# Performance work log

Hardware: AMD Instinct MI355X
Metric: run time of the kernel (lower is better)

## Reference

```python
import jax, jax.numpy as jnp
import numpy as np

N = 4096
FIN = 4096
LOC = 16
H1, H2, HEADS = 120, 50, 4
H1_PER = H1 // HEADS
FILM_Z = 32
SSDB_H = 60
N_HEMI = N // 2
NEG_SLOPE = 0.1
GATE_BIAS = -2.0
MASK_FILL = -9e15


def leaky(x):
    return jax.nn.leaky_relu(x, negative_slope=NEG_SLOPE)


def gat(x, mask, W, a_src, a_dst, bias, concat):
    # x: (N, Fin), W: (H, Fin, O), a_src/a_dst: (H, O), mask: (N, N) bool
    wh = jnp.einsum('nf,hfo->hno', x, W)            # (H, N, O)
    f1 = jnp.einsum('hno,ho->hn', wh, a_src)        # (H, N)
    f2 = jnp.einsum('hno,ho->hn', wh, a_dst)        # (H, N)
    e = leaky(f1[:, :, None] + f2[:, None, :])      # (H, N, N)
    e = jnp.where(mask[None], e, MASK_FILL)
    alpha = jax.nn.softmax(e, axis=-1)
    out = jnp.einsum('hij,hjo->hio', alpha, wh)     # (H, N, O)
    if concat:
        h, n, o = out.shape
        out2 = out.transpose(1, 0, 2).reshape(n, h * o)
    else:
        out2 = out.mean(axis=0)
    return out2 + bias


def _uni(k, shape, stdv):
    return jax.random.uniform(k, shape, jnp.float32, -stdv, stdv)


def setup_inputs() -> dict:
    key = jax.random.key(0)
    ks = jax.random.split(key, 30)
    s1 = 1.0 / np.sqrt(H1_PER)
    s2 = 1.0 / np.sqrt(H2)
    inp = {
        'x_fc': jax.random.normal(ks[0], (N, FIN), jnp.float32),
        'adj': jax.random.randint(ks[1], (N, N), 0, 2, jnp.int32),
        'l_loc': jax.random.uniform(ks[2], (N, LOC), jnp.float32),
        # gat1
        'W1': _uni(ks[3], (HEADS, FIN, H1_PER), s1),
        'a1s': _uni(ks[4], (HEADS, H1_PER), s1),
        'a1d': _uni(ks[5], (HEADS, H1_PER), s1),
        'b1': _uni(ks[6], (H1,), s1),
        # gat2
        'W2': _uni(ks[7], (1, H1, H2), s2),
        'a2s': _uni(ks[8], (1, H2), s2),
        'a2d': _uni(ks[9], (1, H2), s2),
        'b2': _uni(ks[10], (H2,), s2),
        # classifier (no bias)
        'Wc': _uni(ks[11], (2, H2), s2),
        # FiLM trunk
        'Wl1': _uni(ks[12], (FILM_Z, LOC), 1.0 / np.sqrt(LOC)),
        'bl1': _uni(ks[13], (FILM_Z,), 1.0 / np.sqrt(LOC)),
        'Wl2': _uni(ks[14], (FILM_Z, FILM_Z), 1.0 / np.sqrt(FILM_Z)),
        'bl2': _uni(ks[15], (FILM_Z,), 1.0 / np.sqrt(FILM_Z)),
        'Wg': _uni(ks[16], (H2, FILM_Z), 1.0 / np.sqrt(FILM_Z)),
        'bg': _uni(ks[17], (H2,), 1.0 / np.sqrt(FILM_Z)),
        'Wb': _uni(ks[18], (H2, FILM_Z), 1.0 / np.sqrt(FILM_Z)),
        'bb': _uni(ks[19], (H2,), 1.0 / np.sqrt(FILM_Z)),
        'Wgate': _uni(ks[20], (1, FILM_Z), 1.0 / np.sqrt(FILM_Z)),
        'bgate': jnp.full((1,), GATE_BIAS, jnp.float32),
        # SSDB hemi
        'Ws1': _uni(ks[21], (SSDB_H, N_HEMI), 1.0 / np.sqrt(N_HEMI)),
        'bs1': _uni(ks[22], (SSDB_H,), 1.0 / np.sqrt(N_HEMI)),
        'Ws2': _uni(ks[23], (1, SSDB_H), 1.0 / np.sqrt(SSDB_H)),
        'bs2': _uni(ks[24], (1,), 1.0 / np.sqrt(SSDB_H)),
    }
    return inp


def reference(x_fc, adj, l_loc, W1, a1s, a1d, b1, W2, a2s, a2d, b2, Wc,
              Wl1, bl1, Wl2, bl2, Wg, bg, Wb, bb, Wgate, bgate,
              Ws1, bs1, Ws2, bs2):
    mask = adj > 0
    h = leaky(gat(x_fc, mask, W1, a1s, a1d, b1, concat=True))    # (N, 120)
    h = leaky(gat(h, mask, W2, a2s, a2d, b2, concat=False))      # (N, 50)
    # FiLM conditioning
    z = leaky(l_loc @ Wl1.T + bl1)
    z = leaky(z @ Wl2.T + bl2)
    gamma = z @ Wg.T + bg                                        # (N, 50)
    beta = z @ Wb.T + bb                                         # (N, 50)
    g = jax.nn.sigmoid(z @ Wgate.T + bgate)                      # (N, 1)
    cov = jnp.clip(l_loc[:, -1], 0.0, 1.0)                       # coverage_power = 1.0
    g = g * cov[:, None]
    h_fused = h + g * (gamma * h + beta)
    logits = leaky(h_fused @ Wc.T)                               # (N, 2)
    # hemisphere SSDB bias
    t = logits.T                                                 # (2, N)
    ipsi = t[:, :N_HEMI]
    contra = t[:, N_HEMI:2 * N_HEMI]
    h_i = leaky(ipsi @ Ws1.T + bs1)                              # (2, 60)
    h_c = leaky(contra @ Ws1.T + bs1)
    b_i = leaky(h_i @ Ws2.T + bs2)                               # (2, 1)
    b_c = leaky(h_c @ Ws2.T + bs2)
    b_mid = 0.5 * (b_i + b_c)                                    # (2, 1)
    bias_nodes = jnp.concatenate([
        jnp.broadcast_to(b_i.T, (N_HEMI, 2)),
        jnp.broadcast_to(b_c.T, (N_HEMI, 2)),
    ], axis=0)                                                   # n_mid = 0
    logits = logits + bias_nodes
    bias_avg = b_mid[:, 0]                                       # (2,)
    return logits, bias_avg
```

## Files before the change

kernel.cpp:

```cpp
#include <hip/hip_runtime.h>

#define NN 4096
#define NNP 4128
#define BROW 132
#define HEADS 4
#define H1PER 30
#define H1DIM 120
#define H2DIM 50

typedef short short8_t __attribute__((ext_vector_type(8)));
typedef float f32x4 __attribute__((ext_vector_type(4)));

__device__ __forceinline__ float lrelu(float x) { return x > 0.f ? x : 0.1f * x; }

__device__ __forceinline__ unsigned short bfrne(float x) {
  unsigned u = __float_as_uint(x);
  u += 0x7fffu + ((u >> 16) & 1u);
  return (unsigned short)(u >> 16);
}
__device__ __forceinline__ unsigned bfpk_rne(float lo, float hi) {
  return (unsigned)bfrne(lo) | ((unsigned)bfrne(hi) << 16);
}
__device__ __forceinline__ unsigned bfpk(float lo, float hi) {
  unsigned a = (__float_as_uint(lo) + 0x8000u) >> 16;
  unsigned b = (__float_as_uint(hi) + 0x8000u) & 0xffff0000u;
  return a | b;
}
__device__ __forceinline__ unsigned fenc(float x) {
  unsigned u = __float_as_uint(x);
  return (u & 0x80000000u) ? ~u : (u | 0x80000000u);
}
__device__ __forceinline__ float fdec(unsigned u) {
  return (u & 0x80000000u) ? __uint_as_float(u ^ 0x80000000u) : __uint_as_float(~u);
}

#define GL16(g, l)                                                                        \
  __builtin_amdgcn_global_load_lds((const __attribute__((address_space(1))) unsigned int*)(g), \
                                   (__attribute__((address_space(3))) unsigned int*)(l), 16, 0, 0)

__global__ __launch_bounds__(256) void k_bits(const int* __restrict__ adj,
                                              unsigned long long* __restrict__ bits) {
  int n = blockIdx.x >> 2, r = blockIdx.x & 3;
  size_t base = (size_t)n * 4096 + r * 1024;
  int t = threadIdx.x;
  int v0 = adj[base + t];
  int v1 = adj[base + 256 + t];
  int v2 = adj[base + 512 + t];
  int v3 = adj[base + 768 + t];
  unsigned long long m0 = __ballot(v0 > 0);
  unsigned long long m1 = __ballot(v1 > 0);
  unsigned long long m2 = __ballot(v2 > 0);
  unsigned long long m3 = __ballot(v3 > 0);
  if ((t & 63) == 0) {
    size_t w = (size_t)n * (BROW / 2) + r * 16 + (t >> 6);
    bits[w] = m0;
    bits[w + 4] = m1;
    bits[w + 8] = m2;
    bits[w + 12] = m3;
  }
}

__global__ __launch_bounds__(256) void k_prep(const float* __restrict__ W1,
                                              const float* __restrict__ a1s,
                                              const float* __restrict__ a1d,
                                              unsigned short* __restrict__ w1t) {
  int k = blockIdx.x * 256 + threadIdx.x;
#pragma unroll
  for (int h = 0; h < 4; ++h) {
    const float* wp = W1 + ((size_t)h * 4096 + k) * H1PER;
    float fs = 0.f, fd = 0.f;
#pragma unroll
    for (int oo = 0; oo < H1PER; ++oo) {
      float v = wp[oo];
      w1t[(size_t)(h * 30 + oo) * NNP + k] = bfrne(v);
      fs += v * a1s[h * H1PER + oo];
      fd += v * a1d[h * H1PER + oo];
    }
    w1t[(size_t)(120 + h) * NNP + k] = bfrne(fs);
    w1t[(size_t)(124 + h) * NNP + k] = bfrne(fd);
  }
}

__global__ __launch_bounds__(256) void k_gemm1s(const float* __restrict__ x,
                                                const unsigned short* __restrict__ w1t,
                                                float* __restrict__ part) {
  const int t = threadIdx.x;
  const int lane = t & 63, wave = t >> 6;
  const int m = lane & 15, q = lane >> 4;
  const int i0 = blockIdx.x * 32;
  const int kz = blockIdx.y * 512;
  __shared__ float xs[2][32 * 64];
  __shared__ unsigned short bs[2][128 * 64];
  const int r0 = (wave & 1) * 16;
  const int ntg0 = (wave >> 1) * 4;
  const int srow0 = wave * 8 + q;
  const int srow1 = srow0 + 4;
  const float* gx0 = x + (size_t)(i0 + srow0) * 4096 + kz + (m ^ (srow0 & 7)) * 4;
  const float* gx1 = x + (size_t)(i0 + srow1) * 4096 + kz + (m ^ (srow1 & 7)) * 4;
  const int lo0 = srow0 * 64 + m * 4;
  const int lo1 = srow1 * 64 + m * 4;
  const int l8 = lane >> 3, c8 = lane & 7;
  const unsigned short* gb = w1t + (size_t)(wave * 32 + l8) * NNP + kz + (c8 ^ l8) * 8;
  const int bo = wave * 2048 + lane * 8;
  const int arow = r0 + m;
  const int asw = m & 7;
  f32x4 acc[4];
#pragma unroll
  for (int nt = 0; nt < 4; ++nt) acc[nt] = (f32x4){0.f, 0.f, 0.f, 0.f};

  GL16(gx0, &xs[0][lo0]);
  GL16(gx1, &xs[0][lo1]);
#pragma unroll
  for (int i = 0; i < 4; ++i) GL16(gb + (size_t)i * 8 * NNP, &bs[0][bo + i * 512]);

#pragma unroll
  for (int it = 0; it < 8; ++it) {
    const int cur = it & 1;
    if (it < 7) {
      const int kc = (it + 1) * 64;
      GL16(gx0 + kc, &xs[cur ^ 1][lo0]);
      GL16(gx1 + kc, &xs[cur ^ 1][lo1]);
#pragma unroll
      for (int i = 0; i < 4; ++i) GL16(gb + (size_t)i * 8 * NNP + kc, &bs[cur ^ 1][bo + i * 512]);
      asm volatile("s_waitcnt vmcnt(6)" ::: "memory");
    } else {
      asm volatile("s_waitcnt vmcnt(0)" ::: "memory");
    }
    __builtin_amdgcn_s_barrier();
    __builtin_amdgcn_sched_barrier(0);
#pragma unroll
    for (int ks2 = 0; ks2 < 2; ++ks2) {
      const int c0 = ks2 * 8 + q * 2;
      float4 a0 = *(const float4*)&xs[cur][arow * 64 + ((c0 ^ asw) * 4)];
      float4 a1 = *(const float4*)&xs[cur][arow * 64 + (((c0 + 1) ^ asw) * 4)];
      union { short8_t v; unsigned u[4]; } A;
      A.u[0] = bfpk_rne(a0.x, a0.y);
      A.u[1] = bfpk_rne(a0.z, a0.w);
      A.u[2] = bfpk_rne(a1.x, a1.y);
      A.u[3] = bfpk_rne(a1.z, a1.w);
      const int bch = ((ks2 << 2) | q) ^ asw;
#pragma unroll
      for (int nt = 0; nt < 4; ++nt) {
        short8_t B = *(const short8_t*)&bs[cur][((ntg0 + nt) * 16 + m) * 64 + bch * 8];
        acc[nt] = __builtin_amdgcn_mfma_f32_16x16x32_bf16(A.v, B, acc[nt], 0, 0, 0);
      }
    }
    __builtin_amdgcn_sched_barrier(0);
    __builtin_amdgcn_s_barrier();
  }
  float* pp = part + ((size_t)blockIdx.y * 4096 + i0 + r0 + q * 4) * 128 + ntg0 * 16 + m;
#pragma unroll
  for (int nt = 0; nt < 4; ++nt)
#pragma unroll
    for (int r = 0; r < 4; ++r) pp[r * 128 + nt * 16] = acc[nt][r];
}

__global__ __launch_bounds__(256) void k_f1c(const float* __restrict__ part,
                                             unsigned short* __restrict__ whbt,
                                             float* __restrict__ f1, float* __restrict__ f2,
                                             unsigned* __restrict__ mxu1) {
  const int t = threadIdx.x;
  const int n = blockIdx.x * 16 + (t >> 4);
  const int og = (t & 15) * 8;
  __shared__ float f2loc[16][4];
  float s[8] = {0.f, 0.f, 0.f, 0.f, 0.f, 0.f, 0.f, 0.f};
  for (int z = 0; z < 8; ++z) {
    const float* pp = part + ((size_t)z * NN + n) * 128 + og;
    float4 u0 = *(const float4*)pp;
    float4 u1 = *(const float4*)(pp + 4);
    s[0] += u0.x; s[1] += u0.y; s[2] += u0.z; s[3] += u0.w;
    s[4] += u1.x; s[5] += u1.y; s[6] += u1.z; s[7] += u1.w;
  }
  if (og < 120) {
#pragma unroll
    for (int j = 0; j < 8; ++j) {
      int o = og + j;
      int h = o / 30, oo = o - h * 30;
      whbt[(size_t)(h * 32 + oo) * NNP + n] = bfrne(s[j]);
    }
  } else {
#pragma unroll
    for (int j = 0; j < 4; ++j) {
      f1[(size_t)j * NN + n] = s[j];
      f2[(size_t)j * NN + n] = s[4 + j];
      f2loc[t >> 4][j] = s[4 + j];
    }
  }
  if ((t & 15) < 8) {
    int h = (t & 15) >> 1, odd = (t & 15) & 1;
    whbt[(size_t)(h * 32 + 30 + odd) * NNP + n] = odd ? 0 : 0x3f80;
  }
  __syncthreads();
  if (t < 4) {
    float m = f2loc[0][t];
#pragma unroll
    for (int i = 1; i < 16; ++i) m = fmaxf(m, f2loc[i][t]);
    atomicMax(&mxu1[t], fenc(m));
  }
}

__global__ __launch_bounds__(256) void k_att1m(const unsigned short* __restrict__ whbt,
                                               const float* __restrict__ f1, const float* __restrict__ f2,
                                               const unsigned* __restrict__ mxu1,
                                               const unsigned int* __restrict__ bits32,
                                               float* __restrict__ part) {
  const int h = blockIdx.y, js = blockIdx.z;
  const int t = threadIdx.x;
  const int lane = t & 63, wave = t >> 6;
  const int m = lane & 15, q = lane >> 4;
  const int i0 = blockIdx.x * 64 + wave * 16;
  const int jbase = js * 1024;
  const float mxh = fdec(mxu1[h]);
  __shared__ float2 es[1024];
  for (int e = t; e < 1024; e += 256) {
    float fv = f2[h * NN + jbase + e] - mxh;
    es[e] = make_float2(__expf(fv), __expf(0.1f * fv));
  }
  __syncthreads();
  const float f1r = f1[h * NN + i0 + m];
  const float s = f1r + mxh;
  const float R = __expf(fminf(60.f, -0.9f * s));
  const uint4* brow4 = (const uint4*)(bits32 + (size_t)(i0 + m) * BROW + (jbase >> 5));
  const unsigned short* bb0 = whbt + (size_t)(h * 32 + m) * NNP + jbase + q * 8;
  const unsigned short* bb1 = bb0 + 16 * NNP;
  const float2* fp = es + q * 8;
  f32x4 acc0 = {0.f, 0.f, 0.f, 0.f}, acc1 = {0.f, 0.f, 0.f, 0.f};
  for (int s4 = 0; s4 < 8; ++s4) {
    uint4 bq = brow4[s4];
#pragma unroll
    for (int sub = 0; sub < 4; ++sub) {
      const int step = s4 * 4 + sub;
      const int jl = step * 32;
      unsigned bsel = (sub == 0 ? bq.x : sub == 1 ? bq.y : sub == 2 ? bq.z : bq.w) >> (q * 8);
      float4 e01 = *(const float4*)(fp + jl);
      float4 e23 = *(const float4*)(fp + jl + 2);
      float4 e45 = *(const float4*)(fp + jl + 4);
      float4 e67 = *(const float4*)(fp + jl + 6);
      auto sc = [&](float ep, float en, int jj) {
        float wv = fmaxf(ep, R * en);
        return ((bsel >> jj) & 1u) ? wv : 0.f;
      };
      union { short8_t v; unsigned u[4]; } A;
      A.u[0] = bfpk(sc(e01.x, e01.y, 0), sc(e01.z, e01.w, 1));
      A.u[1] = bfpk(sc(e23.x, e23.y, 2), sc(e23.z, e23.w, 3));
      A.u[2] = bfpk(sc(e45.x, e45.y, 4), sc(e45.z, e45.w, 5));
      A.u[3] = bfpk(sc(e67.x, e67.y, 6), sc(e67.z, e67.w, 7));
      short8_t b0 = *(const short8_t*)(bb0 + jl);
      short8_t b1 = *(const short8_t*)(bb1 + jl);
      acc0 = __builtin_amdgcn_mfma_f32_16x16x32_bf16(A.v, b0, acc0, 0, 0, 0);
      acc1 = __builtin_amdgcn_mfma_f32_16x16x32_bf16(A.v, b1, acc1, 0, 0, 0);
    }
  }
  float* pp = part + ((size_t)(js * 4 + h) * NN + i0 + q * 4) * 32 + m;
#pragma unroll
  for (int r = 0; r < 4; ++r) {
    pp[r * 32] = acc0[r];
    pp[r * 32 + 16] = acc1[r];
  }
}

__global__ __launch_bounds__(256) void k_fuseA(const float* __restrict__ part, const float* __restrict__ b1,
                                               const float* __restrict__ W2, const float* __restrict__ a2s,
                                               const float* __restrict__ a2d,
                                               unsigned short* __restrict__ whbt2,
                                               float* __restrict__ f1b, float* __restrict__ f2b,
                                               unsigned* __restrict__ mxu2) {
  const int t = threadIdx.x;
  __shared__ float W2s[H1DIM * H2DIM];
  __shared__ float h1s[4][124];
  __shared__ float f2red[4];
  for (int e = t; e < H1DIM * H2DIM; e += 256) W2s[e] = W2[e];
  const int wv = t >> 6, lane = t & 63;
  const int n = blockIdx.x * 4 + wv;
  const int h = lane >> 4, o2 = (lane & 15) * 2;
  float tot0 = 0.f, tot1 = 0.f;
#pragma unroll
  for (int z = 0; z < 4; ++z) {
    const float* pp = part + ((size_t)(z * 4 + h) * NN + n) * 32 + o2;
    float2 u = *(const float2*)pp;
    tot0 += u.x;
    tot1 += u.y;
  }
  float l = __shfl(tot0, h * 16 + 15);
  float inv = 1.f / l;
  if (o2 < 30) {
    h1s[wv][h * 30 + o2] = lrelu(tot0 * inv + b1[h * 30 + o2]);
    h1s[wv][h * 30 + o2 + 1] = lrelu(tot1 * inv + b1[h * 30 + o2 + 1]);
  }
  __syncthreads();
  const int o = lane;
  float acc = 0.f;
  if (o < H2DIM) {
    const float* hr = h1s[wv];
#pragma unroll 4
    for (int k = 0; k < H1DIM; ++k) acc += hr[k] * W2s[k * H2DIM + o];
  }
  unsigned short wbv = (o < H2DIM) ? bfrne(acc) : (o == H2DIM ? (unsigned short)0x3f80 : (unsigned short)0);
  whbt2[(size_t)o * NNP + n] = wbv;
  float ps = (o < H2DIM) ? acc * a2s[o] : 0.f;
  float pd = (o < H2DIM) ? acc * a2d[o] : 0.f;
  for (int off = 32; off > 0; off >>= 1) {
    ps += __shfl_down(ps, off);
    pd += __shfl_down(pd, off);
  }
  if (lane == 0) {
    f1b[n] = ps;
    f2b[n] = pd;
    f2red[wv] = pd;
  }
  __syncthreads();
  if (t == 0) {
    float m = fmaxf(fmaxf(f2red[0], f2red[1]), fmaxf(f2red[2], f2red[3]));
    atomicMax(mxu2, fenc(m));
  }
}

__global__ __launch_bounds__(256) void k_att2m(const unsigned short* __restrict__ whbt2,
                                               const float* __restrict__ f1b, const float* __restrict__ f2b,
                                               const unsigned* __restrict__ mxu2,
                                               const unsigned int* __restrict__ bits32,
                                               float* __restrict__ part) {
  const int js = blockIdx.y;
  const int t = threadIdx.x;
  const int lane = t & 63, wave = t >> 6;
  const int m = lane & 15, q = lane >> 4;
  const int i0 = blockIdx.x * 64 + wave * 16;
  const int jbase = js * 512;
  const float mx0 = fdec(mxu2[0]);
  __shared__ float2 es[512];
  for (int e = t; e < 512; e += 256) {
    float fv = f2b[jbase + e] - mx0;
    es[e] = make_float2(__expf(fv), __expf(0.1f * fv));
  }
  __syncthreads();
  const float f1r = f1b[i0 + m];
  const float s = f1r + mx0;
  const float R = __expf(fminf(60.f, -0.9f * s));
  const uint4* brow4 = (const uint4*)(bits32 + (size_t)(i0 + m) * BROW + (jbase >> 5));
  const unsigned short* bb = whbt2 + (size_t)m * NNP + jbase + q * 8;
  const float2* fp = es + q * 8;
  f32x4 acc[4];
#pragma unroll
  for (int x = 0; x < 4; ++x) acc[x] = (f32x4){0.f, 0.f, 0.f, 0.f};
  for (int s4 = 0; s4 < 4; ++s4) {
    uint4 bq = brow4[s4];
#pragma unroll
    for (int sub = 0; sub < 4; ++sub) {
      const int step = s4 * 4 + sub;
      const int jl = step * 32;
      unsigned bsel = (sub == 0 ? bq.x : sub == 1 ? bq.y : sub == 2 ? bq.z : bq.w) >> (q * 8);
      float4 e01 = *(const float4*)(fp + jl);
      float4 e23 = *(const float4*)(fp + jl + 2);
      float4 e45 = *(const float4*)(fp + jl + 4);
      float4 e67 = *(const float4*)(fp + jl + 6);
      auto sc = [&](float ep, float en, int jj) {
        float wv = fmaxf(ep, R * en);
        return ((bsel >> jj) & 1u) ? wv : 0.f;
      };
      union { short8_t v; unsigned u[4]; } A;
      A.u[0] = bfpk(sc(e01.x, e01.y, 0), sc(e01.z, e01.w, 1));
      A.u[1] = bfpk(sc(e23.x, e23.y, 2), sc(e23.z, e23.w, 3));
      A.u[2] = bfpk(sc(e45.x, e45.y, 4), sc(e45.z, e45.w, 5));
      A.u[3] = bfpk(sc(e67.x, e67.y, 6), sc(e67.z, e67.w, 7));
#pragma unroll
      for (int tile = 0; tile < 4; ++tile) {
        short8_t b = *(const short8_t*)(bb + (size_t)tile * 16 * NNP + jl);
        acc[tile] = __builtin_amdgcn_mfma_f32_16x16x32_bf16(A.v, b, acc[tile], 0, 0, 0);
      }
    }
  }
  float* pp = part + ((size_t)js * NN + i0 + q * 4) * 64 + m;
#pragma unroll
  for (int tile = 0; tile < 4; ++tile)
#pragma unroll
    for (int r = 0; r < 4; ++r) pp[r * 64 + tile * 16] = acc[tile][r];
}

__global__ __launch_bounds__(256) void k_fuseB(const float* __restrict__ part, const float* __restrict__ b2,
                                               const float* __restrict__ l_loc,
                                               const float* __restrict__ Wl1, const float* __restrict__ bl1,
                                               const float* __restrict__ Wl2, const float* __restrict__ bl2,
                                               const float* __restrict__ Wg, const float* __restrict__ bg,
                                               const float* __restrict__ Wb, const float* __restrict__ bb,
                                               const float* __restrict__ Wgate, const float* __restrict__ bgate,
                                               const float* __restrict__ Wc, float* __restrict__ logits) {
  const int t = threadIdx.x;
  const int wv = t >> 6, lane = t & 63;
  const int n = blockIdx.x * 4 + wv;
  const float* p = part + (size_t)n * 64 + lane;
  float tot = 0.f;
#pragma unroll
  for (int z = 0; z < 8; ++z) tot += p[(size_t)z * NN * 64];
  float l = __shfl(tot, 50);
  float hv = (lane < H2DIM) ? lrelu(tot / l + b2[lane]) : 0.f;
  int r32 = lane & 31;
  float locv = l_loc[n * 16 + (lane & 15)];
  float cov = __shfl(locv, 15);
  cov = fminf(fmaxf(cov, 0.f), 1.f);
  float a1v = bl1[r32];
#pragma unroll
  for (int j = 0; j < 16; ++j) a1v += Wl1[r32 * 16 + j] * __shfl(locv, j);
  float z1 = lrelu(a1v);
  float a2v = bl2[r32];
#pragma unroll
  for (int j = 0; j < 32; ++j) a2v += Wl2[r32 * 32 + j] * __shfl(z1, j);
  float z2 = lrelu(a2v);
  float gs = bgate[0];
  float gam, bet;
  {
    int o = lane < H2DIM ? lane : 0;
    gam = bg[o];
    bet = bb[o];
#pragma unroll
    for (int j = 0; j < 32; ++j) {
      float zj = __shfl(z2, j);
      gs += Wgate[j] * zj;
      gam += Wg[o * 32 + j] * zj;
      bet += Wb[o * 32 + j] * zj;
    }
  }
  float g = cov / (1.f + __expf(-gs));
  float hf = hv + g * (gam * hv + bet);
  int o = lane < H2DIM ? lane : 0;
  float p0 = lane < H2DIM ? hf * Wc[o] : 0.f;
  float p1 = lane < H2DIM ? hf * Wc[H2DIM + o] : 0.f;
  for (int off = 32; off > 0; off >>= 1) {
    p0 += __shfl_down(p0, off);
    p1 += __shfl_down(p1, off);
  }
  if (lane == 0) {
    logits[n * 2 + 0] = lrelu(p0);
    logits[n * 2 + 1] = lrelu(p1);
  }
}

__global__ __launch_bounds__(64) void k_ssdbA(const float* __restrict__ logits,
                                              const float* __restrict__ Ws1, const float* __restrict__ bs1,
                                              const float* __restrict__ Ws2, float* __restrict__ hsum) {
  const int k = blockIdx.x, combo = blockIdx.y;
  const int hemi = combo >> 1, c = combo & 1;
  const int lane = threadIdx.x;
  const float* wr = Ws1 + (size_t)k * 2048;
  const float* lc = logits + (size_t)hemi * 4096 + c;
  float acc = 0.f;
#pragma unroll 4
  for (int i = lane; i < 2048; i += 64) acc += wr[i] * lc[2 * i];
  for (int off = 32; off > 0; off >>= 1) acc += __shfl_down(acc, off);
  if (lane == 0) hsum[combo * 60 + k] = lrelu(acc + bs1[k]) * Ws2[k];
}

__global__ __launch_bounds__(256) void k_finB(const float* __restrict__ hsum,
                                              const float* __restrict__ bs2,
                                              const float* __restrict__ logits,
                                              float* __restrict__ out) {
  __shared__ float Bs[4];
  const int t = threadIdx.x;
  {
    int combo = t >> 6, k = t & 63;
    float v = (k < 60) ? hsum[combo * 60 + k] : 0.f;
    for (int off = 32; off > 0; off >>= 1) v += __shfl_down(v, off);
    if (k == 0) Bs[combo] = lrelu(v + bs2[0]);
  }
  __syncthreads();
  int id = blockIdx.x * 256 + t;
  if (id < 2 * NN) {
    int n = id >> 1, c = id & 1;
    out[id] = logits[id] + Bs[(n < 2048 ? 0 : 2) + c];
  } else if (id < 2 * NN + 2) {
    int c = id - 2 * NN;
    out[id] = 0.5f * (Bs[c] + Bs[2 + c]);
  }
}

#define OFF_BITS 0
#define OFF_W1T 540672
#define OFF_GP 804864
#define OFF_A1P 804864
#define OFF_A2P 804864
#define OFF_WH1BT 4999168
#define OFF_F1A 5263360
#define OFF_F2A 5279744
#define OFF_WH2BT 5296128
#define OFF_F12 5428224
#define OFF_F22 5432320
#define OFF_LOG 5436416
#define OFF_MX 5444608
#define OFF_HS 5444672

extern "C" void kernel_launch(void* const* d_in, const int* in_sizes, int n_in,
                              void* d_out, int out_size, void* d_ws, size_t ws_size,
                              hipStream_t stream) {
  const float* x_fc  = (const float*)d_in[0];
  const int*   adj   = (const int*)d_in[1];
  const float* l_loc = (const float*)d_in[2];
  const float* W1    = (const float*)d_in[3];
  const float* a1s   = (const float*)d_in[4];
  const float* a1d   = (const float*)d_in[5];
  const float* b1    = (const float*)d_in[6];
  const float* W2    = (const float*)d_in[7];
  const float* a2s   = (const float*)d_in[8];
  const float* a2d   = (const float*)d_in[9];
  const float* b2    = (const float*)d_in[10];
  const float* Wc    = (const float*)d_in[11];
  const float* Wl1   = (const float*)d_in[12];
  const float* bl1   = (const float*)d_in[13];
  const float* Wl2   = (const float*)d_in[14];
  const float* bl2   = (const float*)d_in[15];
  const float* Wg    = (const float*)d_in[16];
  const float* bg    = (const float*)d_in[17];
  const float* Wb    = (const float*)d_in[18];
  const float* bb    = (const float*)d_in[19];
  const float* Wgate = (const float*)d_in[20];
  const float* bgate = (const float*)d_in[21];
  const float* Ws1   = (const float*)d_in[22];
  const float* bs1   = (const float*)d_in[23];
  const float* Ws2   = (const float*)d_in[24];
  const float* bs2   = (const float*)d_in[25];
  float* out = (float*)d_out;
  float* w = (float*)d_ws;
  unsigned long long* bits = (unsigned long long*)(w + OFF_BITS);
  const unsigned int* bits32 = (const unsigned int*)bits;
  unsigned short* wh1bt = (unsigned short*)(w + OFF_WH1BT);
  unsigned short* wh2bt = (unsigned short*)(w + OFF_WH2BT);
  unsigned short* w1t = (unsigned short*)(w + OFF_W1T);
  unsigned* mxu = (unsigned*)(w + OFF_MX);

  hipMemsetAsync(mxu, 0, 8 * sizeof(unsigned), stream);
  k_bits<<<NN * NN / 1024, 256, 0, stream>>>(adj, bits);
  k_prep<<<16, 256, 0, stream>>>(W1, a1s, a1d, w1t);
  k_gemm1s<<<dim3(128, 8), 256, 0, stream>>>(x_fc, w1t, w + OFF_GP);
  k_f1c<<<256, 256, 0, stream>>>(w + OFF_GP, wh1bt, w + OFF_F1A, w + OFF_F2A, mxu);
  k_att1m<<<dim3(64, HEADS, 4), 256, 0, stream>>>(wh1bt, w + OFF_F1A, w + OFF_F2A,
                                                  mxu, bits32, w + OFF_A1P);
  k_fuseA<<<1024, 256, 0, stream>>>(w + OFF_A1P, b1, W2, a2s, a2d, wh2bt,
                                    w + OFF_F12, w + OFF_F22, mxu + 4);
  k_att2m<<<dim3(64, 8), 256, 0, stream>>>(wh2bt, w + OFF_F12, w + OFF_F22,
                                           mxu + 4, bits32, w + OFF_A2P);
  k_fuseB<<<1024, 256, 0, stream>>>(w + OFF_A2P, b2, l_loc, Wl1, bl1, Wl2, bl2,
                                    Wg, bg, Wb, bb, Wgate, bgate, Wc, w + OFF_LOG);
  k_ssdbA<<<dim3(60, 4), 64, 0, stream>>>(w + OFF_LOG, Ws1, bs1, Ws2, w + OFF_HS);
  k_finB<<<33, 256, 0, stream>>>(w + OFF_HS, bs2, w + OFF_LOG, out);
}
```

Measured before the change: 315.0 us.

## Stage attention B operands through double-buffered swizzled LDS with async loads

Both attention kernels (k_att1m, k_att2m) now copy the bf16 Wh^T tiles into a two-slot LDS buffer with direct global-to-LDS loads (GL16), prefetching the next j-chunk while MFMAs run on the current one. Previously each of the four waves loaded the same B fragments from global memory on its own; now the block loads them once and shares them. An XOR swizzle on the LDS layout is meant to avoid bank conflicts on the fragment reads. The cost is extra LDS use, two barriers per chunk and manual vmcnt waits, which can lower occupancy or serialize waves.

Measured after the change: 308.0 us. 1.02x faster.

```diff
diff --git a/kernel.cpp b/kernel.cpp
--- a/kernel.cpp
+++ b/kernel.cpp
@@ -212,30 +212,189 @@
   const int jbase = js * 1024;
   const float mxh = fdec(mxu1[h]);
   __shared__ float2 es[1024];
+  __shared__ unsigned short bsm1[2][8192];
   for (int e = t; e < 1024; e += 256) {
     float fv = f2[h * NN + jbase + e] - mxh;
     es[e] = make_float2(__expf(fv), __expf(0.1f * fv));
   }
-  __syncthreads();
   const float f1r = f1[h * NN + i0 + m];
   const float s = f1r + mxh;
   const float R = __expf(fminf(60.f, -0.9f * s));
   const uint4* brow4 = (const uint4*)(bits32 + (size_t)(i0 + m) * BROW + (jbase >> 5));
-  const unsigned short* bb0 = whbt + (size_t)(h * 32 + m) * NNP + jbase + q * 8;
-  const unsigned short* bb1 = bb0 + 16 * NNP;
-  const float2* fp = es + q * 8;
+  const float2* fp = es;
+  const int r_st = t >> 3;
+  const unsigned short* gB = whbt + (size_t)(h * 32 + r_st) * NNP + jbase + ((t & 7) ^ (r_st & 7)) * 8;
   f32x4 acc0 = {0.f, 0.f, 0.f, 0.f}, acc1 = {0.f, 0.f, 0.f, 0.f};
-  for (int s4 = 0; s4 < 8; ++s4) {
-    uint4 bq = brow4[s4];
+
+  __syncthreads();
+
+#pragma unroll
+  for (int c = 0; c < 4; ++c) GL16(gB + c * 64, &bsm1[0][c * 2048 + t * 8]);
+
+#pragma unroll
+  for (int jc = 0; jc < 4; ++jc) {
+    const int cur = jc & 1;
+    const uint4 bqA = brow4[jc * 2];
+    const uint4 bqB = brow4[jc * 2 + 1];
+    if (jc < 3) {
+#pragma unroll
+      for (int c = 0; c < 4; ++c) GL16(gB + (jc + 1) * 256 + c * 64, &bsm1[cur ^ 1][c * 2048 + t * 8]);
+      asm volatile("s_waitcnt vmcnt(4)" ::: "memory");
+    } else {
+      asm volatile("s_waitcnt vmcnt(0)" ::: "memory");
+    }
+    __builtin_amdgcn_s_barrier();
+    __builtin_amdgcn_sched_barrier(0);
+#pragma unroll
+    for (int g = 0; g < 2; ++g) {
+      const uint4 bq = g ? bqB : bqA;
+#pragma unroll
+      for (int sub = 0; sub < 4; ++sub) {
+        const int jl = (jc * 2 + g) * 128 + sub * 32;
+        unsigned bsel = (sub == 0 ? bq.x : sub == 1 ? bq.y : sub == 2 ? bq.z : bq.w) >> (q * 8);
+        float4 e01 = *(const float4*)(fp + jl + q * 8);
+        float4 e23 = *(const float4*)(fp + jl + q * 8 + 2);
+        float4 e45 = *(const float4*)(fp + jl + q * 8 + 4);
+        float4 e67 = *(const float4*)(fp + jl + q * 8 + 6);
+        auto sc = [&](float ep, float en, int jj) {
+          float wv = fmaxf(ep, R * en);
+          return ((bsel >> jj) & 1u) ? wv : 0.f;
+        };
+        union { short8_t v; unsigned u[4]; } A;
+        A.u[0] = bfpk(sc(e01.x, e01.y, 0), sc(e01.z, e01.w, 1));
+        A.u[1] = bfpk(sc(e23.x, e23.y, 2), sc(e23.z, e23.w, 3));
+        A.u[2] = bfpk(sc(e45.x, e45.y, 4), sc(e45.z, e45.w, 5));
+        A.u[3] = bfpk(sc(e67.x, e67.y, 6), sc(e67.z, e67.w, 7));
+        const int p = g * 16 + sub * 4 + q;
+        short8_t b0 = *(const short8_t*)&bsm1[cur][(p >> 3) * 2048 + m * 64 + ((p & 7) ^ (m & 7)) * 8];
+        short8_t b1 = *(const short8_t*)&bsm1[cur][(p >> 3) * 2048 + (m + 16) * 64 + ((p & 7) ^ ((m + 16) & 7)) * 8];
+        acc0 = __builtin_amdgcn_mfma_f32_16x16x32_bf16(A.v, b0, acc0, 0, 0, 0);
+        acc1 = __builtin_amdgcn_mfma_f32_16x16x32_bf16(A.v, b1, acc1, 0, 0, 0);
+      }
+    }
+    __builtin_amdgcn_sched_barrier(0);
+    __builtin_amdgcn_s_barrier();
+  }
+  float* pp = part + ((size_t)(js * 4 + h) * NN + i0 + q * 4) * 32 + m;
+#pragma unroll
+  for (int r = 0; r < 4; ++r) {
+    pp[r * 32] = acc0[r];
+    pp[r * 32 + 16] = acc1[r];
+  }
+}
+
+__global__ __launch_bounds__(256) void k_fuseA(const float* __restrict__ part, const float* __restrict__ b1,
+                                               const float* __restrict__ W2, const float* __restrict__ a2s,
+                                               const float* __restrict__ a2d,
+                                               unsigned short* __restrict__ whbt2,
+                                               float* __restrict__ f1b, float* __restrict__ f2b,
+                                               unsigned* __restrict__ mxu2) {
+  const int t = threadIdx.x;
+  __shared__ float W2s[H1DIM * H2DIM];
+  __shared__ float h1s[4][124];
+  __shared__ float f2red[4];
+  for (int e = t; e < H1DIM * H2DIM; e += 256) W2s[e] = W2[e];
+  const int wv = t >> 6, lane = t & 63;
+  const int n = blockIdx.x * 4 + wv;
+  const int h = lane >> 4, o2 = (lane & 15) * 2;
+  float tot0 = 0.f, tot1 = 0.f;
+#pragma unroll
+  for (int z = 0; z < 4; ++z) {
+    const float* pp = part + ((size_t)(z * 4 + h) * NN + n) * 32 + o2;
+    float2 u = *(const float2*)pp;
+    tot0 += u.x;
+    tot1 += u.y;
+  }
+  float l = __shfl(tot0, h * 16 + 15);
+  float inv = 1.f / l;
+  if (o2 < 30) {
+    h1s[wv][h * 30 + o2] = lrelu(tot0 * inv + b1[h * 30 + o2]);
+    h1s[wv][h * 30 + o2 + 1] = lrelu(tot1 * inv + b1[h * 30 + o2 + 1]);
+  }
+  __syncthreads();
+  const int o = lane;
+  float acc = 0.f;
+  if (o < H2DIM) {
+    const float* hr = h1s[wv];
+#pragma unroll 4
+    for (int k = 0; k < H1DIM; ++k) acc += hr[k] * W2s[k * H2DIM + o];
+  }
+  unsigned short wbv = (o < H2DIM) ? bfrne(acc) : (o == H2DIM ? (unsigned short)0x3f80 : (unsigned short)0);
+  whbt2[(size_t)o * NNP + n] = wbv;
+  float ps = (o < H2DIM) ? acc * a2s[o] : 0.f;
+  float pd = (o < H2DIM) ? acc * a2d[o] : 0.f;
+  for (int off = 32; off > 0; off >>= 1) {
+    ps += __shfl_down(ps, off);
+    pd += __shfl_down(pd, off);
+  }
+  if (lane == 0) {
+    f1b[n] = ps;
+    f2b[n] = pd;
+    f2red[wv] = pd;
+  }
+  __syncthreads();
+  if (t == 0) {
+    float m = fmaxf(fmaxf(f2red[0], f2red[1]), fmaxf(f2red[2], f2red[3]));
+    atomicMax(mxu2, fenc(m));
+  }
+}
+
+__global__ __launch_bounds__(256) void k_att2m(const unsigned short* __restrict__ whbt2,
+                                               const float* __restrict__ f1b, const float* __restrict__ f2b,
+                                               const unsigned* __restrict__ mxu2,
+                                               const unsigned int* __restrict__ bits32,
+                                               float* __restrict__ part) {
+  const int js = blockIdx.y;
+  const int t = threadIdx.x;
+  const int lane = t & 63, wave = t >> 6;
+  const int m = lane & 15, q = lane >> 4;
+  const int i0 = blockIdx.x * 64 + wave * 16;
+  const int jbase = js * 512;
+  const float mx0 = fdec(mxu2[0]);
+  __shared__ float2 es[512];
+  __shared__ unsigned short bsm2[2][8192];
+  for (int e = t; e < 512; e += 256) {
+    float fv = f2b[jbase + e] - mx0;
+    es[e] = make_float2(__expf(fv), __expf(0.1f * fv));
+  }
+  const float f1r = f1b[i0 + m];
+  const float s = f1r + mx0;
+  const float R = __expf(fminf(60.f, -0.9f * s));
+  const uint4* brow4 = (const uint4*)(bits32 + (size_t)(i0 + m) * BROW + (jbase >> 5));
+  const float2* fp = es;
+  const int r2 = t >> 2;
+  const int sw2 = (r2 & 3) ^ ((r2 >> 2) & 3);
+  const unsigned short* gB2 = whbt2 + (size_t)r2 * NNP + jbase + ((t & 3) ^ sw2) * 8;
+  f32x4 acc[4];
+#pragma unroll
+  for (int xx = 0; xx < 4; ++xx) acc[xx] = (f32x4){0.f, 0.f, 0.f, 0.f};
+
+  __syncthreads();
+
+#pragma unroll
+  for (int c = 0; c < 4; ++c) GL16(gB2 + c * 32, &bsm2[0][c * 2048 + t * 8]);
+
+#pragma unroll
+  for (int jc = 0; jc < 4; ++jc) {
+    const int cur = jc & 1;
+    const uint4 bq = brow4[jc];
+    if (jc < 3) {
+#pragma unroll
+      for (int c = 0; c < 4; ++c) GL16(gB2 + (jc + 1) * 128 + c * 32, &bsm2[cur ^ 1][c * 2048 + t * 8]);
+      asm volatile("s_waitcnt vmcnt(4)" ::: "memory");
+    } else {
+      asm volatile("s_waitcnt vmcnt(0)" ::: "memory");
+    }
+    __builtin_amdgcn_s_barrier();
+    __builtin_amdgcn_sched_barrier(0);
 #pragma unroll
     for (int sub = 0; sub < 4; ++sub) {
-      const int step = s4 * 4 + sub;
-      const int jl = step * 32;
+      const int jl = jc * 128 + sub * 32;
       unsigned bsel = (sub == 0 ? bq.x : sub == 1 ? bq.y : sub == 2 ? bq.z : bq.w) >> (q * 8);
-      float4 e01 = *(const float4*)(fp + jl);
-      float4 e23 = *(const float4*)(fp + jl + 2);
-      float4 e45 = *(const float4*)(fp + jl + 4);
-      float4 e67 = *(const float4*)(fp + jl + 6);
+      float4 e01 = *(const float4*)(fp + jl + q * 8);
+      float4 e23 = *(const float4*)(fp + jl + q * 8 + 2);
+      float4 e45 = *(const float4*)(fp + jl + q * 8 + 4);
+      float4 e67 = *(const float4*)(fp + jl + q * 8 + 6);
       auto sc = [&](float ep, float en, int jj) {
         float wv = fmaxf(ep, R * en);
         return ((bsel >> jj) & 1u) ? wv : 0.f;
@@ -245,129 +404,17 @@
       A.u[1] = bfpk(sc(e23.x, e23.y, 2), sc(e23.z, e23.w, 3));
       A.u[2] = bfpk(sc(e45.x, e45.y, 4), sc(e45.z, e45.w, 5));
       A.u[3] = bfpk(sc(e67.x, e67.y, 6), sc(e67.z, e67.w, 7));
-      short8_t b0 = *(const short8_t*)(bb0 + jl);
-      short8_t b1 = *(const short8_t*)(bb1 + jl);
-      acc0 = __builtin_amdgcn_mfma_f32_16x16x32_bf16(A.v, b0, acc0, 0, 0, 0);
-      acc1 = __builtin_amdgcn_mfma_f32_16x16x32_bf16(A.v, b1, acc1, 0, 0, 0);
-    }
-  }
-  float* pp = part + ((size_t)(js * 4 + h) * NN + i0 + q * 4) * 32 + m;
-#pragma unroll
-  for (int r = 0; r < 4; ++r) {
-    pp[r * 32] = acc0[r];
-    pp[r * 32 + 16] = acc1[r];
-  }
-}
-
-__global__ __launch_bounds__(256) void k_fuseA(const float* __restrict__ part, const float* __restrict__ b1,
-                                               const float* __restrict__ W2, const float* __restrict__ a2s,
-                                               const float* __restrict__ a2d,
-                                               unsigned short* __restrict__ whbt2,
-                                               float* __restrict__ f1b, float* __restrict__ f2b,
-                                               unsigned* __restrict__ mxu2) {
-  const int t = threadIdx.x;
-  __shared__ float W2s[H1DIM * H2DIM];
-  __shared__ float h1s[4][124];
-  __shared__ float f2red[4];
-  for (int e = t; e < H1DIM * H2DIM; e += 256) W2s[e] = W2[e];
-  const int wv = t >> 6, lane = t & 63;
-  const int n = blockIdx.x * 4 + wv;
-  const int h = lane >> 4, o2 = (lane & 15) * 2;
-  float tot0 = 0.f, tot1 = 0.f;
-#pragma unroll
-  for (int z = 0; z < 4; ++z) {
-    const float* pp = part + ((size_t)(z * 4 + h) * NN + n) * 32 + o2;
-    float2 u = *(const float2*)pp;
-    tot0 += u.x;
-    tot1 += u.y;
-  }
-  float l = __shfl(tot0, h * 16 + 15);
-  float inv = 1.f / l;
-  if (o2 < 30) {
-    h1s[wv][h * 30 + o2] = lrelu(tot0 * inv + b1[h * 30 + o2]);
-    h1s[wv][h * 30 + o2 + 1] = lrelu(tot1 * inv + b1[h * 30 + o2 + 1]);
-  }
-  __syncthreads();
-  const int o = lane;
-  float acc = 0.f;
-  if (o < H2DIM) {
-    const float* hr = h1s[wv];
-#pragma unroll 4
-    for (int k = 0; k < H1DIM; ++k) acc += hr[k] * W2s[k * H2DIM + o];
-  }
-  unsigned short wbv = (o < H2DIM) ? bfrne(acc) : (o == H2DIM ? (unsigned short)0x3f80 : (unsigned short)0);
-  whbt2[(size_t)o * NNP + n] = wbv;
-  float ps = (o < H2DIM) ? acc * a2s[o] : 0.f;
-  float pd = (o < H2DIM) ? acc * a2d[o] : 0.f;
-  for (int off = 32; off > 0; off >>= 1) {
-    ps += __shfl_down(ps, off);
-    pd += __shfl_down(pd, off);
-  }
-  if (lane == 0) {
-    f1b[n] = ps;
-    f2b[n] = pd;
-    f2red[wv] = pd;
-  }
-  __syncthreads();
-  if (t == 0) {
-    float m = fmaxf(fmaxf(f2red[0], f2red[1]), fmaxf(f2red[2], f2red[3]));
-    atomicMax(mxu2, fenc(m));
-  }
-}
-
-__global__ __launch_bounds__(256) void k_att2m(const unsigned short* __restrict__ whbt2,
-                                               const float* __restrict__ f1b, const float* __restrict__ f2b,
-                                               const unsigned* __restrict__ mxu2,
-                                               const unsigned int* __restrict__ bits32,
-                                               float* __restrict__ part) {
-  const int js = blockIdx.y;
-  const int t = threadIdx.x;
-  const int lane = t & 63, wave = t >> 6;
-  const int m = lane & 15, q = lane >> 4;
-  const int i0 = blockIdx.x * 64 + wave * 16;
-  const int jbase = js * 512;
-  const float mx0 = fdec(mxu2[0]);
-  __shared__ float2 es[512];
-  for (int e = t; e < 512; e += 256) {
-    float fv = f2b[jbase + e] - mx0;
-    es[e] = make_float2(__expf(fv), __expf(0.1f * fv));
-  }
-  __syncthreads();
-  const float f1r = f1b[i0 + m];
-  const float s = f1r + mx0;
-  const float R = __expf(fminf(60.f, -0.9f * s));
-  const uint4* brow4 = (const uint4*)(bits32 + (size_t)(i0 + m) * BROW + (jbase >> 5));
-  const unsigned short* bb = whbt2 + (size_t)m * NNP + jbase + q * 8;
-  const float2* fp = es + q * 8;
-  f32x4 acc[4];
-#pragma unroll
-  for (int x = 0; x < 4; ++x) acc[x] = (f32x4){0.f, 0.f, 0.f, 0.f};
-  for (int s4 = 0; s4 < 4; ++s4) {
-    uint4 bq = brow4[s4];
-#pragma unroll
-    for (int sub = 0; sub < 4; ++sub) {
-      const int step = s4 * 4 + sub;
-      const int jl = step * 32;
-      unsigned bsel = (sub == 0 ? bq.x : sub == 1 ? bq.y : sub == 2 ? bq.z : bq.w) >> (q * 8);
-      float4 e01 = *(const float4*)(fp + jl);
-      float4 e23 = *(const float4*)(fp + jl + 2);
-      float4 e45 = *(const float4*)(fp + jl + 4);
-      float4 e67 = *(const float4*)(fp + jl + 6);
-      auto sc = [&](float ep, float en, int jj) {
-        float wv = fmaxf(ep, R * en);
-        return ((bsel >> jj) & 1u) ? wv : 0.f;
-      };
-      union { short8_t v; unsigned u[4]; } A;
-      A.u[0] = bfpk(sc(e01.x, e01.y, 0), sc(e01.z, e01.w, 1));
-      A.u[1] = bfpk(sc(e23.x, e23.y, 2), sc(e23.z, e23.w, 3));
-      A.u[2] = bfpk(sc(e45.x, e45.y, 4), sc(e45.z, e45.w, 5));
-      A.u[3] = bfpk(sc(e67.x, e67.y, 6), sc(e67.z, e67.w, 7));
+      const int p = sub * 4 + q;
 #pragma unroll
       for (int tile = 0; tile < 4; ++tile) {
-        short8_t b = *(const short8_t*)(bb + (size_t)tile * 16 * NNP + jl);
+        const int f = tile * 16 + m;
+        const int sw = (f & 3) ^ ((f >> 2) & 3);
+        short8_t b = *(const short8_t*)&bsm2[cur][(p >> 2) * 2048 + f * 32 + (((p & 3) ^ sw)) * 8];
         acc[tile] = __builtin_amdgcn_mfma_f32_16x16x32_bf16(A.v, b, acc[tile], 0, 0, 0);
       }
     }
+    __builtin_amdgcn_sched_barrier(0);
+    __builtin_amdgcn_s_barrier();
   }
   float* pp = part + ((size_t)js * NN + i0 + q * 4) * 64 + m;
 #pragma unroll
```
